# Optimization experiments

Measured on AMD Instinct MI355X. Metric: run time of the kernel, lower is better.

The kernel has to match this reference:

```python
import jax, jax.numpy as jnp
import numpy as np

NGRAM_NS = (2, 3)  # window sizes of the 2 hidden layers ('2,3,4' -> num_hidden_layers=2)


def _ngram(x, n):
    # x: (b, s, d) -> (b, s, n, d); window i holds x[i:i+n], zero-padded at the end
    s = x.shape[1]
    xp = jnp.pad(x, ((0, 0), (0, n - 1), (0, 0)))
    return jnp.stack([xp[:, j:j + s] for j in range(n)], axis=2)


def _mixture_weighted(r, i, w):
    # r,i: (..., n, d); w: (..., n, 1) -> weighted sum of outer products |phi><phi|
    w = w[..., 0]
    Rr = jnp.einsum('...nd,...ne,...n->...de', r, r, w) + jnp.einsum('...nd,...ne,...n->...de', i, i, w)
    Ri = jnp.einsum('...nd,...ne,...n->...de', i, r, w) - jnp.einsum('...nd,...ne,...n->...de', r, i, w)
    return Rr, Ri


def _normalize_complex(vr, vi):
    n = jnp.sqrt(jnp.sum(vr * vr + vi * vi, axis=-1, keepdims=True))
    return vr / n, vi / n


def _quad_form(Rr, Ri, vr, vi):
    # <v_k| rho |v_k> for each measurement vector v_k; Rr,Ri: (..., d, d); vr,vi: (k, d)
    ar = jnp.einsum('...de,ke->...dk', Rr, vr) - jnp.einsum('...de,ke->...dk', Ri, vi)
    ai = jnp.einsum('...de,ke->...dk', Rr, vi) + jnp.einsum('...de,ke->...dk', Ri, vr)
    out_r = jnp.einsum('kd,...dk->...k', vr, ar) + jnp.einsum('kd,...dk->...k', vi, ai)
    out_i = jnp.einsum('kd,...dk->...k', vr, ai) - jnp.einsum('kd,...dk->...k', vi, ar)
    return out_r, out_i


def setup_inputs() -> dict:
    key = jax.random.key(0)
    ks = jax.random.split(key, 9)
    V, D, B, S, U, L = 50000, 100, 16, 128, 100, 2
    return {
        'input_seq': jax.random.randint(ks[0], (B, S), 0, V),
        'amp_table': jax.random.normal(ks[1], (V, D), jnp.float32),
        'phase_table': jax.random.uniform(ks[2], (V, D), jnp.float32, -np.pi, np.pi),
        'proj_kernel_r': jax.random.normal(ks[3], (L, D, D), jnp.float32),
        'proj_kernel_i': jax.random.normal(ks[4], (L, D, D), jnp.float32),
        'meas_kernel_r': jax.random.normal(ks[5], (U, D), jnp.float32),
        'meas_kernel_i': jax.random.normal(ks[6], (U, D), jnp.float32),
        'dense_w': jax.random.normal(ks[7], (U, 2), jnp.float32) * 0.1,
        'dense_b': jnp.zeros((2,), jnp.float32),
    }


def reference(input_seq, amp_table, phase_table, proj_kernel_r, proj_kernel_i,
              meas_kernel_r, meas_kernel_i, dense_w, dense_b):
    # ComplexEmbedding
    amp = amp_table[input_seq]      # (b, s, d)
    phase = phase_table[input_seq]  # (b, s, d)
    # L2Norm / L2Normalization
    weights = jnp.linalg.norm(amp, axis=-1, keepdims=True)  # (b, s, 1)
    amp = amp / weights
    # ComplexMultiply: state = amp * e^{i phase}
    seq_r = amp * jnp.cos(phase)
    seq_i = amp * jnp.sin(phase)
    for li, n in enumerate(NGRAM_NS):
        gr = _ngram(seq_r, n)                                  # (b, s, n, d)
        gi = _ngram(seq_i, n)
        gw = jax.nn.softmax(_ngram(weights, n), axis=1)        # Softmax(dim=1) as in torch code
        Rr, Ri = _mixture_weighted(gr, gi, gw)                 # (b, s, d, d)
        vr, vi = _normalize_complex(proj_kernel_r[li], proj_kernel_i[li])
        seq_r, seq_i = _quad_form(Rr, Ri, vr, vi)              # (b, s, d)
    # Final mixture over the sequence dim with the raw L2-norm weights
    Rr, Ri = _mixture_weighted(seq_r, seq_i, weights)          # (b, d, d)
    vr, vi = _normalize_complex(meas_kernel_r, meas_kernel_i)
    probs, _ = _quad_form(Rr, Ri, vr, vi)                      # (b, units) real part of Tr(rho P_k)
    return probs @ dense_w + dense_b
```

## Files before the change

### kernel.cpp

```cpp
#include <hip/hip_runtime.h>
#include <math.h>

#define NB 16
#define SS 128
#define DD 100
#define KK 100
#define T_TILE 8
#define P_HALO 11
#define NTILES 16
#define NT 768
#define NWAVES 12
#define CH_D4 5
#define NCHUNK 5

__device__ __forceinline__ float dot4(const float4 a, const float4 b) {
  return a.x * b.x + a.y * b.y + a.z * b.z + a.w * b.w;
}

template<int MODE>
__device__ __forceinline__ void accum_pair(
    const float4* __restrict__ vtb,
    const float4 (*__restrict__ bxr)[25], const float4 (*__restrict__ bxi)[25],
    int p0, int p1, bool a0, bool a1, int k, int c,
    float& r0a, float& i0a, float& r1a, float& i1a, float& n0)
{
#pragma unroll
  for (int r = 0; r < CH_D4; ++r) {
    const int d4 = c * CH_D4 + r;
    const float4 vr4 = vtb[r * KK + k];
    const float4 vi4 = vtb[500 + r * KK + k];
    n0 += dot4(vr4, vr4) + dot4(vi4, vi4);
    if (a0) {
      const float4 x4 = bxr[p0][d4];
      if (MODE == 0) {
        const float4 z4 = bxi[p0][d4];
        r0a += dot4(vr4, x4) + dot4(vi4, z4);
        i0a += dot4(vr4, z4) - dot4(vi4, x4);
      } else {
        r0a += dot4(vr4, x4);
        i0a += dot4(vi4, x4);
      }
    }
    if (a1) {
      const float4 x4 = bxr[p1][d4];
      if (MODE == 0) {
        const float4 z4 = bxi[p1][d4];
        r1a += dot4(vr4, x4) + dot4(vi4, z4);
        i1a += dot4(vr4, z4) - dot4(vi4, x4);
      } else {
        r1a += dot4(vr4, x4);
        i1a += dot4(vi4, x4);
      }
    }
  }
}

template<int MODE>
__device__ __forceinline__ void run_stage(
    const float* __restrict__ gvr, const float* __restrict__ gvi,
    float4 (*__restrict__ vt)[1000],
    const float4 (*__restrict__ bxr)[25], const float4 (*__restrict__ bxi)[25],
    float* __restrict__ mflat, float2* __restrict__ y2flat,
    float* __restrict__ invvn, const int nslots,
    const int tid, const int lane, const int wid)
{
  const int e0 = tid;
  const int e1 = tid + NT;
  const int p0 = e0 / 500, rm0 = e0 % 500, r0_ = rm0 / 100, k0_ = rm0 % 100;
  const int p1 = e1 / 500, rm1 = e1 % 500, r1_ = rm1 / 100, k1_ = rm1 % 100;
  const float* g0 = (p0 ? gvi : gvr) + k0_ * DD + 4 * r0_;
  const float* g1 = (p1 ? gvi : gvr) + k1_ * DD + 4 * r1_;

  float4 pv0, pv1;
  pv0 = *(const float4*)(g0);
  if (e1 < 1000) pv1 = *(const float4*)(g1);
  vt[0][e0] = pv0;
  if (e1 < 1000) vt[0][e1] = pv1;
  __syncthreads();

  const int s0 = wid, s1 = wid + NWAVES;
  float a0r = 0.f, a0i = 0.f, a1r = 0.f, a1i = 0.f, n0 = 0.f;
  const int kk = (s0 & 1) * 50 + lane;
  const int pp0 = s0 >> 1, pp1 = s1 >> 1;
  const bool act0 = (s0 < nslots), act1 = (s1 < nslots);

  for (int c = 0; c < NCHUNK; ++c) {
    const int buf = c & 1;
    if (c + 1 < NCHUNK) {
      pv0 = *(const float4*)(g0 + 4 * CH_D4 * (c + 1));
      if (e1 < 1000) pv1 = *(const float4*)(g1 + 4 * CH_D4 * (c + 1));
    }
    if (lane < 50)
      accum_pair<MODE>(vt[buf], bxr, bxi, pp0, pp1, act0, act1, kk, c,
                       a0r, a0i, a1r, a1i, n0);
    if (c + 1 < NCHUNK) {
      const int nb = buf ^ 1;
      vt[nb][e0] = pv0;
      if (e1 < 1000) vt[nb][e1] = pv1;
    }
    __syncthreads();
  }

  if (lane < 50) {
    const float rcp = 1.0f / n0;
    if (act0) {
      if (MODE == 0) mflat[pp0 * KK + kk] = (a0r * a0r + a0i * a0i) * rcp;
      else           y2flat[pp0 * KK + kk] = make_float2(a0r, a0i);
    }
    if (act1) {
      if (MODE == 0) mflat[pp1 * KK + kk] = (a1r * a1r + a1i * a1i) * rcp;
      else           y2flat[pp1 * KK + kk] = make_float2(a1r, a1i);
    }
    if (wid < 2) invvn[kk] = rcp;
  }
}

__global__ __launch_bounds__(NT) void k_fused(
    const int* __restrict__ seq,
    const float* __restrict__ ampT, const float* __restrict__ phT,
    const float* __restrict__ pkr, const float* __restrict__ pki,
    const float* __restrict__ mkr, const float* __restrict__ mki,
    float* __restrict__ part)
{
  __shared__ float4 vt[2][1000];
  __shared__ float4 xr4[P_HALO][25];
  __shared__ float4 xi4[P_HALO][25];
  __shared__ float4 m4[P_HALO][25];
  __shared__ float2 y2[P_HALO][KK];
  __shared__ float es[SS];
  __shared__ float wnl[SS];
  __shared__ float invvn[KK];
  __shared__ float redw[NWAVES];
  __shared__ float sc[3];

  const int tid  = threadIdx.x;
  const int lane = tid & 63;
  const int wid  = tid >> 6;
  const int bt   = blockIdx.x;
  const int b    = bt >> 4;
  const int tile = bt & 15;
  const int t0   = tile * T_TILE;
  const int sb   = b * SS;

  if (tid < 4 * SS) {
    const int t = tid >> 2, q = tid & 3;
    const int row = seq[sb + t];
    const float* ap = ampT + (long)row * DD + q;
    float s = 0.f;
#pragma unroll
    for (int i = 0; i < 25; ++i) { const float a = ap[4*i]; s += a * a; }
    s += __shfl_xor(s, 1, 64);
    s += __shfl_xor(s, 2, 64);
    if (q == 0) { const float nrm = sqrtf(s); wnl[t] = nrm; es[t] = expf(nrm); }
  }
  __syncthreads();

  {
    float v = (tid < SS) ? es[tid] : 0.f;
    for (int m = 32; m; m >>= 1) v += __shfl_xor(v, m, 64);
    if (lane == 0) redw[wid] = v;
  }
  for (int idx = tid; idx < P_HALO * 25; idx += NT) {
    const int p = idx / 25, d4 = idx % 25;
    const int tp = t0 + p;
    float4 o_r = {0.f, 0.f, 0.f, 0.f}, o_i = {0.f, 0.f, 0.f, 0.f};
    if (tp < SS) {
      const int row = seq[sb + tp];
      const float4 a4 = *(const float4*)(ampT + (long)row * DD + 4 * d4);
      const float4 p4 = *(const float4*)(phT  + (long)row * DD + 4 * d4);
      const float inv = 1.0f / wnl[tp];
      float sv, cv;
      sincosf(p4.x, &sv, &cv); o_r.x = a4.x * inv * cv; o_i.x = a4.x * inv * sv;
      sincosf(p4.y, &sv, &cv); o_r.y = a4.y * inv * cv; o_i.y = a4.y * inv * sv;
      sincosf(p4.z, &sv, &cv); o_r.z = a4.z * inv * cv; o_i.z = a4.z * inv * sv;
      sincosf(p4.w, &sv, &cv); o_r.w = a4.w * inv * cv; o_i.w = a4.w * inv * sv;
    }
    xr4[p][d4] = o_r;
    xi4[p][d4] = o_i;
  }
  __syncthreads();
  if (tid == 0) {
    float E = 0.f;
    for (int w = 0; w < NWAVES; ++w) E += redw[w];
    sc[0] = E;
    sc[1] = E - es[0] + 1.0f;
    sc[2] = E - es[0] - es[1] + 2.0f;
  }
  __syncthreads();

  run_stage<0>(pkr, pki, vt, xr4, xi4, (float*)m4, nullptr, invvn,
               2 * P_HALO, tid, lane, wid);
  __syncthreads();

  run_stage<1>(pkr + DD * DD, pki + DD * DD, vt, m4, m4, nullptr,
               (float2*)y2, invvn, 2 * P_HALO, tid, lane, wid);
  __syncthreads();

  {
    const float E = sc[0], Z1 = sc[1];
    for (int idx = tid; idx < 10 * KK; idx += NT) {
      const int p = idx / KK, k = idx - p * KK;
      const int t = t0 + p;
      const float w0 = ((t     < SS) ? es[t]     : 1.f) / E;
      const float w1 = ((t + 1 < SS) ? es[t + 1] : 1.f) / Z1;
      const float2 ya = y2[p][k], yb = y2[p + 1][k];
      const float ar = w0 * ya.x + w1 * yb.x;
      const float ai = w0 * ya.y + w1 * yb.y;
      ((float*)m4)[p * KK + k] = (ar * ar + ai * ai) * invvn[k];
    }
  }
  __syncthreads();

  run_stage<1>(mkr, mki, vt, m4, m4, nullptr,
               (float2*)y2, invvn, 20, tid, lane, wid);
  __syncthreads();

  {
    const float E = sc[0], Z1 = sc[1], Z2 = sc[2];
    for (int idx = tid; idx < T_TILE * KK; idx += NT) {
      const int p = idx / KK, k = idx - p * KK;
      const int t = t0 + p;
      const float w0 = es[t] / E;
      const float w1 = ((t + 1 < SS) ? es[t + 1] : 1.f) / Z1;
      const float w2 = ((t + 2 < SS) ? es[t + 2] : 1.f) / Z2;
      const float2 ya = y2[p][k], yb = y2[p + 1][k], yc = y2[p + 2][k];
      const float qr = w0 * ya.x + w1 * yb.x + w2 * yc.x;
      const float qi = w0 * ya.y + w1 * yb.y + w2 * yc.y;
      ((float*)m4)[p * KK + k] = wnl[t] * (qr * qr + qi * qi) * invvn[k];
    }
  }
  __syncthreads();
  if (tid < KK) {
    float s = 0.f;
#pragma unroll
    for (int p = 0; p < T_TILE; ++p) s += ((float*)m4)[p * KK + tid];
    part[bt * KK + tid] = s;
  }
}

__global__ __launch_bounds__(128) void k_out(
    const float* __restrict__ part, const float* __restrict__ dw,
    const float* __restrict__ db, float* __restrict__ out)
{
  __shared__ float pr[KK];
  const int b = blockIdx.x, tid = threadIdx.x;
  if (tid < KK) {
    float s = 0.f;
#pragma unroll
    for (int q = 0; q < NTILES; ++q) s += part[(b * NTILES + q) * KK + tid];
    pr[tid] = s;
  }
  __syncthreads();
  if (tid < 2) {
    float s = db[tid];
    for (int k = 0; k < KK; ++k) s += pr[k] * dw[k * 2 + tid];
    out[b * 2 + tid] = s;
  }
}

extern "C" void kernel_launch(void* const* d_in, const int* in_sizes, int n_in,
                              void* d_out, int out_size, void* d_ws, size_t ws_size,
                              hipStream_t stream) {
  const int*   seq  = (const int*)d_in[0];
  const float* ampT = (const float*)d_in[1];
  const float* phT  = (const float*)d_in[2];
  const float* pkr  = (const float*)d_in[3];
  const float* pki  = (const float*)d_in[4];
  const float* mkr  = (const float*)d_in[5];
  const float* mki  = (const float*)d_in[6];
  const float* dw   = (const float*)d_in[7];
  const float* db   = (const float*)d_in[8];
  float* out  = (float*)d_out;
  float* part = (float*)d_ws;

  k_fused<<<NB * NTILES, NT, 0, stream>>>(seq, ampT, phT, pkr, pki, mkr, mki, part);
  k_out  <<<NB,          128, 0, stream>>>(part, dw, db, out);
}
```

Measured before the change: 34.24 us.

## Register-block stage matvecs over positions and split d-reduction across waves

Each wave now handles a quarter of the d4 chunks (h) and four positions (g) for both k halves, so each loaded projection vector is reused across four positions and two k values held in registers. Partial sums from the four d-slices are reduced through shared memory that reuses the vt buffer. The stage-2 n-gram softmax combine is fused into the stage's epilogue, removing a separate pass. In exchange there are extra barriers and shared-memory round trips for the cross-wave reduction, and each wave keeps more accumulator registers live.

```diff
diff --git a/kernel.cpp b/kernel.cpp
--- a/kernel.cpp
+++ b/kernel.cpp
@@ -10,59 +10,21 @@
 #define NTILES 16
 #define NT 768
 #define NWAVES 12
-#define CH_D4 5
-#define NCHUNK 5
 
 __device__ __forceinline__ float dot4(const float4 a, const float4 b) {
   return a.x * b.x + a.y * b.y + a.z * b.z + a.w * b.w;
 }
 
-template<int MODE>
-__device__ __forceinline__ void accum_pair(
-    const float4* __restrict__ vtb,
-    const float4 (*__restrict__ bxr)[25], const float4 (*__restrict__ bxi)[25],
-    int p0, int p1, bool a0, bool a1, int k, int c,
-    float& r0a, float& i0a, float& r1a, float& i1a, float& n0)
-{
-#pragma unroll
-  for (int r = 0; r < CH_D4; ++r) {
-    const int d4 = c * CH_D4 + r;
-    const float4 vr4 = vtb[r * KK + k];
-    const float4 vi4 = vtb[500 + r * KK + k];
-    n0 += dot4(vr4, vr4) + dot4(vi4, vi4);
-    if (a0) {
-      const float4 x4 = bxr[p0][d4];
-      if (MODE == 0) {
-        const float4 z4 = bxi[p0][d4];
-        r0a += dot4(vr4, x4) + dot4(vi4, z4);
-        i0a += dot4(vr4, z4) - dot4(vi4, x4);
-      } else {
-        r0a += dot4(vr4, x4);
-        i0a += dot4(vi4, x4);
-      }
-    }
-    if (a1) {
-      const float4 x4 = bxr[p1][d4];
-      if (MODE == 0) {
-        const float4 z4 = bxi[p1][d4];
-        r1a += dot4(vr4, x4) + dot4(vi4, z4);
-        i1a += dot4(vr4, z4) - dot4(vi4, x4);
-      } else {
-        r1a += dot4(vr4, x4);
-        i1a += dot4(vi4, x4);
-      }
-    }
-  }
-}
-
-template<int MODE>
+template<int MODE, int CM, int PMAXF, int PMAXC>
 __device__ __forceinline__ void run_stage(
     const float* __restrict__ gvr, const float* __restrict__ gvi,
     float4 (*__restrict__ vt)[1000],
     const float4 (*__restrict__ bxr)[25], const float4 (*__restrict__ bxi)[25],
     float* __restrict__ mflat, float2* __restrict__ y2flat,
-    float* __restrict__ invvn, const int nslots,
-    const int tid, const int lane, const int wid)
+    float* __restrict__ invvn,
+    const float* __restrict__ es, const float* __restrict__ sc,
+    const int tid, const int lane, const int h, const int g,
+    const bool act, const int t0)
 {
   const int e0 = tid;
   const int e1 = tid + NT;
@@ -78,22 +40,52 @@
   if (e1 < 1000) vt[0][e1] = pv1;
   __syncthreads();
 
-  const int s0 = wid, s1 = wid + NWAVES;
-  float a0r = 0.f, a0i = 0.f, a1r = 0.f, a1i = 0.f, n0 = 0.f;
-  const int kk = (s0 & 1) * 50 + lane;
-  const int pp0 = s0 >> 1, pp1 = s1 >> 1;
-  const bool act0 = (s0 < nslots), act1 = (s1 < nslots);
-
-  for (int c = 0; c < NCHUNK; ++c) {
+  float ar[4][2] = {{0.f,0.f},{0.f,0.f},{0.f,0.f},{0.f,0.f}};
+  float ai[4][2] = {{0.f,0.f},{0.f,0.f},{0.f,0.f},{0.f,0.f}};
+  float n0 = 0.f, n1 = 0.f;
+  const int k0 = lane;
+
+  for (int c = 0; c < 5; ++c) {
     const int buf = c & 1;
-    if (c + 1 < NCHUNK) {
-      pv0 = *(const float4*)(g0 + 4 * CH_D4 * (c + 1));
-      if (e1 < 1000) pv1 = *(const float4*)(g1 + 4 * CH_D4 * (c + 1));
-    }
-    if (lane < 50)
-      accum_pair<MODE>(vt[buf], bxr, bxi, pp0, pp1, act0, act1, kk, c,
-                       a0r, a0i, a1r, a1i, n0);
-    if (c + 1 < NCHUNK) {
+    if (c + 1 < 5) {
+      pv0 = *(const float4*)(g0 + 20 * (c + 1));
+      if (e1 < 1000) pv1 = *(const float4*)(g1 + 20 * (c + 1));
+    }
+    if (act) {
+      const float4* vb = vt[buf];
+#pragma unroll
+      for (int r = 0; r < 5; ++r) {
+        const int d4 = 5 * c + r;
+        if ((d4 & 3) == h) {
+          const float4 Vr0 = vb[r * 100 + k0];
+          const float4 Vr1 = vb[r * 100 + 50 + k0];
+          const float4 Vi0 = vb[500 + r * 100 + k0];
+          const float4 Vi1 = vb[500 + r * 100 + 50 + k0];
+          n0 += dot4(Vr0, Vr0) + dot4(Vi0, Vi0);
+          n1 += dot4(Vr1, Vr1) + dot4(Vi1, Vi1);
+#pragma unroll
+          for (int e = 0; e < 4; ++e) {
+            const int p = 4 * g + e;
+            if (p <= PMAXF) {
+              const float4 xr = bxr[p][d4];
+              if (MODE == 0) {
+                const float4 xi = bxi[p][d4];
+                ar[e][0] += dot4(Vr0, xr) + dot4(Vi0, xi);
+                ai[e][0] += dot4(Vr0, xi) - dot4(Vi0, xr);
+                ar[e][1] += dot4(Vr1, xr) + dot4(Vi1, xi);
+                ai[e][1] += dot4(Vr1, xi) - dot4(Vi1, xr);
+              } else {
+                ar[e][0] += dot4(Vr0, xr);
+                ai[e][0] += dot4(Vi0, xr);
+                ar[e][1] += dot4(Vr1, xr);
+                ai[e][1] += dot4(Vi1, xr);
+              }
+            }
+          }
+        }
+      }
+    }
+    if (c + 1 < 5) {
       const int nb = buf ^ 1;
       vt[nb][e0] = pv0;
       if (e1 < 1000) vt[nb][e1] = pv1;
@@ -101,18 +93,76 @@
     __syncthreads();
   }
 
-  if (lane < 50) {
-    const float rcp = 1.0f / n0;
-    if (act0) {
-      if (MODE == 0) mflat[pp0 * KK + kk] = (a0r * a0r + a0i * a0i) * rcp;
-      else           y2flat[pp0 * KK + kk] = make_float2(a0r, a0i);
-    }
-    if (act1) {
-      if (MODE == 0) mflat[pp1 * KK + kk] = (a1r * a1r + a1i * a1i) * rcp;
-      else           y2flat[pp1 * KK + kk] = make_float2(a1r, a1i);
-    }
-    if (wid < 2) invvn[kk] = rcp;
-  }
+  float4* partlp = &vt[0][0];
+  float2* nrmp   = (float2*)(&vt[0][0] + 1200);
+  if (h < 2 && act) {
+#pragma unroll
+    for (int e = 0; e < 4; ++e) {
+      const int p = 4 * g + e;
+      if (p <= PMAXF)
+        partlp[h * 600 + p * 50 + lane] =
+            make_float4(ar[e][0], ai[e][0], ar[e][1], ai[e][1]);
+    }
+    if (g == 0) nrmp[h * 50 + lane] = make_float2(n0, n1);
+  }
+  __syncthreads();
+  if (h >= 2 && act) {
+    const int j = h - 2;
+#pragma unroll
+    for (int e = 0; e < 4; ++e) {
+      const int p = 4 * g + e;
+      if (p <= PMAXF) {
+        float4 s = partlp[j * 600 + p * 50 + lane];
+        s.x += ar[e][0]; s.y += ai[e][0]; s.z += ar[e][1]; s.w += ai[e][1];
+        partlp[j * 600 + p * 50 + lane] = s;
+      }
+    }
+    if (g == 0) {
+      float2 q = nrmp[j * 50 + lane];
+      q.x += n0; q.y += n1;
+      nrmp[j * 50 + lane] = q;
+    }
+  }
+  __syncthreads();
+
+  if (h == 0 && act) {
+    const float2 qa = nrmp[lane], qb = nrmp[50 + lane];
+    const float iv0 = 1.f / (qa.x + qb.x);
+    const float iv1 = 1.f / (qa.y + qb.y);
+#pragma unroll
+    for (int e = 0; e < 4; ++e) {
+      const int p = 4 * g + e;
+      if (p <= PMAXC) {
+        float4 s = partlp[p * 50 + lane];
+        {
+          const float4 s2 = partlp[600 + p * 50 + lane];
+          s.x += s2.x; s.y += s2.y; s.z += s2.z; s.w += s2.w;
+        }
+        if (CM == 1) {
+          mflat[p * KK + lane]      = (s.x * s.x + s.y * s.y) * iv0;
+          mflat[p * KK + 50 + lane] = (s.z * s.z + s.w * s.w) * iv1;
+        } else if (CM == 2) {
+          float4 u = partlp[(p + 1) * 50 + lane];
+          {
+            const float4 u2 = partlp[600 + (p + 1) * 50 + lane];
+            u.x += u2.x; u.y += u2.y; u.z += u2.z; u.w += u2.w;
+          }
+          const int t = t0 + p;
+          const float w0 = ((t     < SS) ? es[t]     : 1.f) / sc[0];
+          const float w1 = ((t + 1 < SS) ? es[t + 1] : 1.f) / sc[1];
+          const float r0 = w0 * s.x + w1 * u.x, i0 = w0 * s.y + w1 * u.y;
+          const float r1 = w0 * s.z + w1 * u.z, i1 = w0 * s.w + w1 * u.w;
+          mflat[p * KK + lane]      = (r0 * r0 + i0 * i0) * iv0;
+          mflat[p * KK + 50 + lane] = (r1 * r1 + i1 * i1) * iv1;
+        } else {
+          y2flat[p * KK + lane]      = make_float2(s.x, s.y);
+          y2flat[p * KK + 50 + lane] = make_float2(s.z, s.w);
+        }
+      }
+    }
+    if (CM == 3 && g == 0) { invvn[lane] = iv0; invvn[50 + lane] = iv1; }
+  }
+  __syncthreads();
 }
 
 __global__ __launch_bounds__(NT) void k_fused(
@@ -136,6 +186,9 @@
   const int tid  = threadIdx.x;
   const int lane = tid & 63;
   const int wid  = tid >> 6;
+  const int h    = wid & 3;
+  const int g    = wid >> 2;
+  const bool act = lane < 50;
   const int bt   = blockIdx.x;
   const int b    = bt >> 4;
   const int tile = bt & 15;
@@ -188,32 +241,13 @@
   }
   __syncthreads();
 
-  run_stage<0>(pkr, pki, vt, xr4, xi4, (float*)m4, nullptr, invvn,
-               2 * P_HALO, tid, lane, wid);
-  __syncthreads();
-
-  run_stage<1>(pkr + DD * DD, pki + DD * DD, vt, m4, m4, nullptr,
-               (float2*)y2, invvn, 2 * P_HALO, tid, lane, wid);
-  __syncthreads();
-
-  {
-    const float E = sc[0], Z1 = sc[1];
-    for (int idx = tid; idx < 10 * KK; idx += NT) {
-      const int p = idx / KK, k = idx - p * KK;
-      const int t = t0 + p;
-      const float w0 = ((t     < SS) ? es[t]     : 1.f) / E;
-      const float w1 = ((t + 1 < SS) ? es[t + 1] : 1.f) / Z1;
-      const float2 ya = y2[p][k], yb = y2[p + 1][k];
-      const float ar = w0 * ya.x + w1 * yb.x;
-      const float ai = w0 * ya.y + w1 * yb.y;
-      ((float*)m4)[p * KK + k] = (ar * ar + ai * ai) * invvn[k];
-    }
-  }
-  __syncthreads();
-
-  run_stage<1>(mkr, mki, vt, m4, m4, nullptr,
-               (float2*)y2, invvn, 20, tid, lane, wid);
-  __syncthreads();
+  run_stage<0, 1, 10, 10>(pkr, pki, vt, xr4, xi4, (float*)m4, nullptr, invvn,
+                          es, sc, tid, lane, h, g, act, t0);
+  run_stage<1, 2, 10, 9>(pkr + DD * DD, pki + DD * DD, vt, m4, m4,
+                         (float*)m4, nullptr, invvn, es, sc,
+                         tid, lane, h, g, act, t0);
+  run_stage<1, 3, 9, 9>(mkr, mki, vt, m4, m4, nullptr, (float2*)y2, invvn,
+                        es, sc, tid, lane, h, g, act, t0);
 
   {
     const float E = sc[0], Z1 = sc[1], Z2 = sc[2];
```

Measured after the change: 59.68 us. +74.3%, slower.

## Pre-transpose projection weights in a prep kernel and read them directly from global memory

Applied to the files above, without the earlier changes.

Adds a small prep kernel that rearranges the projection and measurement matrices into a float4 layout indexed by (d-chunk, k) in workspace. The fused kernel then reads these weights straight from global/L2 instead of staging them through double-buffered shared memory with per-chunk barriers. This drops the shared-memory staging, 18 barriers and the 32KB LDS buffer, which may raise occupancy. In exchange it adds a third kernel launch and relies on cache hits for the repeated weight reads across the 256 blocks.

```diff
diff --git a/kernel.cpp b/kernel.cpp
--- a/kernel.cpp
+++ b/kernel.cpp
@@ -10,119 +10,93 @@
 #define NTILES 16
 #define NT 768
 #define NWAVES 12
-#define CH_D4 5
-#define NCHUNK 5
 
 __device__ __forceinline__ float dot4(const float4 a, const float4 b) {
   return a.x * b.x + a.y * b.y + a.z * b.z + a.w * b.w;
 }
 
+__global__ __launch_bounds__(512) void k_prep(
+    const float* __restrict__ pkr, const float* __restrict__ pki,
+    const float* __restrict__ mkr, const float* __restrict__ mki,
+    float4* __restrict__ Vst)
+{
+  const int g = blockIdx.x * 512 + threadIdx.x;
+  if (g >= 15000) return;
+  const int s    = g / 5000;
+  const int rm   = g - s * 5000;
+  const int part = rm / 2500;
+  const int rm2  = rm - part * 2500;
+  const int r    = rm2 / 100;
+  const int k    = rm2 - r * 100;
+  const float* src;
+  if (s == 0)      src = part ? pki : pkr;
+  else if (s == 1) src = (part ? pki : pkr) + DD * DD;
+  else             src = part ? mki : mkr;
+  Vst[g] = *(const float4*)(src + k * DD + 4 * r);
+}
+
 template<int MODE>
-__device__ __forceinline__ void accum_pair(
-    const float4* __restrict__ vtb,
-    const float4 (*__restrict__ bxr)[25], const float4 (*__restrict__ bxi)[25],
-    int p0, int p1, bool a0, bool a1, int k, int c,
-    float& r0a, float& i0a, float& r1a, float& i1a, float& n0)
-{
-#pragma unroll
-  for (int r = 0; r < CH_D4; ++r) {
-    const int d4 = c * CH_D4 + r;
-    const float4 vr4 = vtb[r * KK + k];
-    const float4 vi4 = vtb[500 + r * KK + k];
-    n0 += dot4(vr4, vr4) + dot4(vi4, vi4);
-    if (a0) {
-      const float4 x4 = bxr[p0][d4];
-      if (MODE == 0) {
-        const float4 z4 = bxi[p0][d4];
-        r0a += dot4(vr4, x4) + dot4(vi4, z4);
-        i0a += dot4(vr4, z4) - dot4(vi4, x4);
-      } else {
-        r0a += dot4(vr4, x4);
-        i0a += dot4(vi4, x4);
-      }
-    }
-    if (a1) {
-      const float4 x4 = bxr[p1][d4];
-      if (MODE == 0) {
-        const float4 z4 = bxi[p1][d4];
-        r1a += dot4(vr4, x4) + dot4(vi4, z4);
-        i1a += dot4(vr4, z4) - dot4(vi4, x4);
-      } else {
-        r1a += dot4(vr4, x4);
-        i1a += dot4(vi4, x4);
-      }
-    }
-  }
-}
-
-template<int MODE>
-__device__ __forceinline__ void run_stage(
-    const float* __restrict__ gvr, const float* __restrict__ gvi,
-    float4 (*__restrict__ vt)[1000],
+__device__ __forceinline__ void run_stage_g(
+    const float4* __restrict__ Vs,
     const float4 (*__restrict__ bxr)[25], const float4 (*__restrict__ bxi)[25],
     float* __restrict__ mflat, float2* __restrict__ y2flat,
     float* __restrict__ invvn, const int nslots,
-    const int tid, const int lane, const int wid)
-{
-  const int e0 = tid;
-  const int e1 = tid + NT;
-  const int p0 = e0 / 500, rm0 = e0 % 500, r0_ = rm0 / 100, k0_ = rm0 % 100;
-  const int p1 = e1 / 500, rm1 = e1 % 500, r1_ = rm1 / 100, k1_ = rm1 % 100;
-  const float* g0 = (p0 ? gvi : gvr) + k0_ * DD + 4 * r0_;
-  const float* g1 = (p1 ? gvi : gvr) + k1_ * DD + 4 * r1_;
-
-  float4 pv0, pv1;
-  pv0 = *(const float4*)(g0);
-  if (e1 < 1000) pv1 = *(const float4*)(g1);
-  vt[0][e0] = pv0;
-  if (e1 < 1000) vt[0][e1] = pv1;
-  __syncthreads();
-
+    const int lane, const int wid)
+{
+  if (lane >= 50) return;
   const int s0 = wid, s1 = wid + NWAVES;
-  float a0r = 0.f, a0i = 0.f, a1r = 0.f, a1i = 0.f, n0 = 0.f;
   const int kk = (s0 & 1) * 50 + lane;
   const int pp0 = s0 >> 1, pp1 = s1 >> 1;
   const bool act0 = (s0 < nslots), act1 = (s1 < nslots);
-
-  for (int c = 0; c < NCHUNK; ++c) {
-    const int buf = c & 1;
-    if (c + 1 < NCHUNK) {
-      pv0 = *(const float4*)(g0 + 4 * CH_D4 * (c + 1));
-      if (e1 < 1000) pv1 = *(const float4*)(g1 + 4 * CH_D4 * (c + 1));
-    }
-    if (lane < 50)
-      accum_pair<MODE>(vt[buf], bxr, bxi, pp0, pp1, act0, act1, kk, c,
-                       a0r, a0i, a1r, a1i, n0);
-    if (c + 1 < NCHUNK) {
-      const int nb = buf ^ 1;
-      vt[nb][e0] = pv0;
-      if (e1 < 1000) vt[nb][e1] = pv1;
-    }
-    __syncthreads();
-  }
-
-  if (lane < 50) {
-    const float rcp = 1.0f / n0;
+  float a0r = 0.f, a0i = 0.f, a1r = 0.f, a1i = 0.f, n0 = 0.f;
+
+#pragma unroll 5
+  for (int r = 0; r < 25; ++r) {
+    const float4 vr4 = Vs[r * 100 + kk];
+    const float4 vi4 = Vs[2500 + r * 100 + kk];
+    n0 += dot4(vr4, vr4) + dot4(vi4, vi4);
     if (act0) {
-      if (MODE == 0) mflat[pp0 * KK + kk] = (a0r * a0r + a0i * a0i) * rcp;
-      else           y2flat[pp0 * KK + kk] = make_float2(a0r, a0i);
+      const float4 x4 = bxr[pp0][r];
+      if (MODE == 0) {
+        const float4 z4 = bxi[pp0][r];
+        a0r += dot4(vr4, x4) + dot4(vi4, z4);
+        a0i += dot4(vr4, z4) - dot4(vi4, x4);
+      } else {
+        a0r += dot4(vr4, x4);
+        a0i += dot4(vi4, x4);
+      }
     }
     if (act1) {
-      if (MODE == 0) mflat[pp1 * KK + kk] = (a1r * a1r + a1i * a1i) * rcp;
-      else           y2flat[pp1 * KK + kk] = make_float2(a1r, a1i);
-    }
-    if (wid < 2) invvn[kk] = rcp;
-  }
+      const float4 x4 = bxr[pp1][r];
+      if (MODE == 0) {
+        const float4 z4 = bxi[pp1][r];
+        a1r += dot4(vr4, x4) + dot4(vi4, z4);
+        a1i += dot4(vr4, z4) - dot4(vi4, x4);
+      } else {
+        a1r += dot4(vr4, x4);
+        a1i += dot4(vi4, x4);
+      }
+    }
+  }
+
+  const float rcp = 1.0f / n0;
+  if (act0) {
+    if (MODE == 0) mflat[pp0 * KK + kk] = (a0r * a0r + a0i * a0i) * rcp;
+    else           y2flat[pp0 * KK + kk] = make_float2(a0r, a0i);
+  }
+  if (act1) {
+    if (MODE == 0) mflat[pp1 * KK + kk] = (a1r * a1r + a1i * a1i) * rcp;
+    else           y2flat[pp1 * KK + kk] = make_float2(a1r, a1i);
+  }
+  if (wid < 2) invvn[kk] = rcp;
 }
 
 __global__ __launch_bounds__(NT) void k_fused(
     const int* __restrict__ seq,
     const float* __restrict__ ampT, const float* __restrict__ phT,
-    const float* __restrict__ pkr, const float* __restrict__ pki,
-    const float* __restrict__ mkr, const float* __restrict__ mki,
+    const float4* __restrict__ Vst,
     float* __restrict__ part)
 {
-  __shared__ float4 vt[2][1000];
   __shared__ float4 xr4[P_HALO][25];
   __shared__ float4 xi4[P_HALO][25];
   __shared__ float4 m4[P_HALO][25];
@@ -188,12 +162,12 @@
   }
   __syncthreads();
 
-  run_stage<0>(pkr, pki, vt, xr4, xi4, (float*)m4, nullptr, invvn,
-               2 * P_HALO, tid, lane, wid);
-  __syncthreads();
-
-  run_stage<1>(pkr + DD * DD, pki + DD * DD, vt, m4, m4, nullptr,
-               (float2*)y2, invvn, 2 * P_HALO, tid, lane, wid);
+  run_stage_g<0>(Vst, xr4, xi4, (float*)m4, nullptr, invvn,
+                 2 * P_HALO, lane, wid);
+  __syncthreads();
+
+  run_stage_g<1>(Vst + 5000, m4, m4, nullptr, (float2*)y2, invvn,
+                 2 * P_HALO, lane, wid);
   __syncthreads();
 
   {
@@ -211,8 +185,8 @@
   }
   __syncthreads();
 
-  run_stage<1>(mkr, mki, vt, m4, m4, nullptr,
-               (float2*)y2, invvn, 20, tid, lane, wid);
+  run_stage_g<1>(Vst + 10000, m4, m4, nullptr, (float2*)y2, invvn,
+                 20, lane, wid);
   __syncthreads();
 
   {
@@ -270,9 +244,13 @@
   const float* mki  = (const float*)d_in[6];
   const float* dw   = (const float*)d_in[7];
   const float* db   = (const float*)d_in[8];
-  float* out  = (float*)d_out;
-  float* part = (float*)d_ws;
-
-  k_fused<<<NB * NTILES, NT, 0, stream>>>(seq, ampT, phT, pkr, pki, mkr, mki, part);
+  float* out = (float*)d_out;
+
+  float*  ws   = (float*)d_ws;
+  float*  part = ws;
+  float4* Vst  = (float4*)(ws + 25600);
+
+  k_prep <<<30,          512, 0, stream>>>(pkr, pki, mkr, mki, Vst);
+  k_fused<<<NB * NTILES, NT,  0, stream>>>(seq, ampT, phT, Vst, part);
   k_out  <<<NB,          128, 0, stream>>>(part, dw, db, out);
 }
```

Result: slower. 52.52 us (+53.4%).
